# Kernel tuning notes

Measured on AMD Instinct MI355X. Metric: run time of the kernel, lower is better.

Reference implementation:

```python
import jax, jax.numpy as jnp
import numpy as np

NUM_MODULES, INP, OUT = 64, 256, 256
B, T = 2048, 64


def setup_inputs() -> dict:
    key = jax.random.key(0)
    k1, k2, k3, k4 = jax.random.split(key, 4)
    x = jax.random.normal(k1, (B, T, INP), dtype=jnp.float32)
    indices = jax.random.randint(k2, (B,), 0, NUM_MODULES)
    # torch.nn.Linear init: U(-1/sqrt(in), 1/sqrt(in)) for both weight and bias
    bound = 1.0 / np.sqrt(INP)
    W = jax.random.uniform(k3, (NUM_MODULES, OUT, INP), minval=-bound, maxval=bound, dtype=jnp.float32)
    b = jax.random.uniform(k4, (NUM_MODULES, OUT), minval=-bound, maxval=bound, dtype=jnp.float32)
    return {"x": x, "indices": indices, "W": W, "b": b}


def reference(x, indices, W, b):
    # Per-sample expert selection: gather each sample's weight/bias, batched matmul.
    Wg = W[indices]            # [B, OUT, INP]
    bg = b[indices]            # [B, OUT]
    y = jnp.einsum("bti,boi->bto", x, Wg) + bg[:, None, :]
    return y
```

## Files before the change

kernel.cpp:

```cpp
#include <hip/hip_runtime.h>
#include <hip/hip_bf16.h>

#define NMOD 64
#define INPD 256
#define OUTD 256
#define BATCH 2048
#define TT 64

typedef __attribute__((ext_vector_type(8))) short short8;
typedef __attribute__((ext_vector_type(4))) float floatx4;

__device__ __forceinline__ unsigned int pack2(float a, float b) {
    union { float f; unsigned int u; } ua, ub; ua.f = a; ub.f = b;
    unsigned int ra = ua.u + 0x7fffu + ((ua.u >> 16) & 1u);
    unsigned int rb = ub.u + 0x7fffu + ((ub.u >> 16) & 1u);
    return (ra >> 16) | (rb & 0xffff0000u);
}

__global__ __launch_bounds__(256) void conv_w_kernel(const float* __restrict__ W,
                                                     uint4* __restrict__ Wp) {
    int gid  = blockIdx.x * 256 + threadIdx.x;
    int lane = gid & 63;
    int frag = (gid >> 6) & 15;
    int ks   = (gid >> 10) & 7;
    int e    = gid >> 13;

    int n = (frag >> 3) * 128 + (frag & 7) * 16 + (lane & 15);
    int k = ks * 32 + (lane >> 4) * 8;

    const float* p = W + ((size_t)e * OUTD + n) * INPD + k;
    float4 v0 = *reinterpret_cast<const float4*>(p);
    float4 v1 = *reinterpret_cast<const float4*>(p + 4);
    Wp[gid] = make_uint4(pack2(v0.x, v0.y), pack2(v0.z, v0.w),
                         pack2(v1.x, v1.y), pack2(v1.z, v1.w));
}

template <bool PRECONV>
__global__ __launch_bounds__(256) void moe_gemm_kernel(
    const float* __restrict__ x, const int* __restrict__ idx,
    const void* __restrict__ Wsrc, const float* __restrict__ bias,
    float* __restrict__ y) {

    __shared__ unsigned short lx[TT * INPD];

    const int b    = blockIdx.x;
    const int tid  = threadIdx.x;
    const int lane = tid & 63;
    const int w    = tid >> 6;
    const int e    = idx[b];
    const int l15  = lane & 15;
    const int kq   = lane >> 4;

    const float4* xin = reinterpret_cast<const float4*>(x + (size_t)b * TT * INPD);
    char* lxc = reinterpret_cast<char*>(lx);
#pragma unroll
    for (int r = 0; r < 16; ++r) {
        int fid  = r * 256 + tid;
        float4 v = xin[fid];
        int t    = fid >> 6;
        int k    = (fid & 63) * 4;
        int byte = t * 512 + ((k * 2) ^ ((t & 7) << 4));
        __builtin_assume((byte & 7) == 0);
        *reinterpret_cast<uint2*>(lxc + byte) = make_uint2(pack2(v.x, v.y), pack2(v.z, v.w));
    }
    __syncthreads();

    floatx4 acc[4][4] = {};

#pragma unroll
    for (int ks = 0; ks < 8; ++ks) {
        short8 af[4];
#pragma unroll
        for (int mi = 0; mi < 4; ++mi) {
            int t    = mi * 16 + l15;
            int byte = t * 512 + ((ks * 64 + kq * 16) ^ ((t & 7) << 4));
            __builtin_assume((byte & 15) == 0);
            af[mi] = *reinterpret_cast<const short8*>(lxc + byte);
        }
        short8 bf[4];
        if (PRECONV) {
            const unsigned short* wp = reinterpret_cast<const unsigned short*>(Wsrc)
                + (((size_t)e * 8 + ks) << 13) + (w << 11) + (lane << 3);
#pragma unroll
            for (int ni = 0; ni < 4; ++ni)
                bf[ni] = *reinterpret_cast<const short8*>(wp + (ni << 9));
        } else {
            const float* Wf = reinterpret_cast<const float*>(Wsrc) + (size_t)e * OUTD * INPD;
#pragma unroll
            for (int ni = 0; ni < 4; ++ni) {
                int n = w * 64 + ni * 16 + l15;
                int k = ks * 32 + kq * 8;
                const float* p = Wf + (size_t)n * INPD + k;
                float4 v0 = *reinterpret_cast<const float4*>(p);
                float4 v1 = *reinterpret_cast<const float4*>(p + 4);
                union { short8 s; uint4 u; } cv;
                cv.u = make_uint4(pack2(v0.x, v0.y), pack2(v0.z, v0.w),
                                  pack2(v1.x, v1.y), pack2(v1.z, v1.w));
                bf[ni] = cv.s;
            }
        }
#pragma unroll
        for (int mi = 0; mi < 4; ++mi)
#pragma unroll
            for (int ni = 0; ni < 4; ++ni)
                acc[mi][ni] = __builtin_amdgcn_mfma_f32_16x16x32_bf16(
                    af[mi], bf[ni], acc[mi][ni], 0, 0, 0);
    }

    float bv[4];
#pragma unroll
    for (int ni = 0; ni < 4; ++ni)
        bv[ni] = bias[e * OUTD + w * 64 + ni * 16 + l15];

    float* yout = y + (size_t)b * TT * OUTD;
#pragma unroll
    for (int mi = 0; mi < 4; ++mi) {
#pragma unroll
        for (int ni = 0; ni < 4; ++ni) {
            int o = w * 64 + ni * 16 + l15;
#pragma unroll
            for (int r = 0; r < 4; ++r) {
                int t = mi * 16 + kq * 4 + r;
                yout[t * OUTD + o] = acc[mi][ni][r] + bv[ni];
            }
        }
    }
}

extern "C" void kernel_launch(void* const* d_in, const int* in_sizes, int n_in,
                              void* d_out, int out_size, void* d_ws, size_t ws_size,
                              hipStream_t stream) {
    const float* x    = (const float*)d_in[0];
    const int*   idx  = (const int*)d_in[1];
    const float* W    = (const float*)d_in[2];
    const float* bias = (const float*)d_in[3];
    float*       y    = (float*)d_out;

    const size_t w_elems      = (size_t)NMOD * OUTD * INPD;
    const size_t w_bf16_bytes = w_elems * sizeof(unsigned short);

    if (ws_size >= w_bf16_bytes) {
        conv_w_kernel<<<(unsigned)(w_elems / 8 / 256), 256, 0, stream>>>(
            W, reinterpret_cast<uint4*>(d_ws));
        moe_gemm_kernel<true><<<BATCH, 256, 0, stream>>>(x, idx, d_ws, bias, y);
    } else {
        moe_gemm_kernel<false><<<BATCH, 256, 0, stream>>>(x, idx, (const void*)W, bias, y);
    }
}
```

Before: 74.78 us.

## Load x directly into MFMA fragments, swap operands for vectorized output stores

Drops the LDS staging of the x tile and the block barrier. Each wave now loads and converts its A fragments from global memory directly, so every wave reloads the full x tile, which leans on L2/L1 for reuse. The MFMA operands are swapped so each lane holds four consecutive output columns, which turns the scalar output stores and bias loads into 16-byte vector accesses. A launch-bounds occupancy hint of 4 blocks is also added.

Measured after the change: 114.8 us. +53.5%, slower.

```diff
diff --git a/kernel.cpp b/kernel.cpp
--- a/kernel.cpp
+++ b/kernel.cpp
@@ -36,12 +36,10 @@
 }
 
 template <bool PRECONV>
-__global__ __launch_bounds__(256) void moe_gemm_kernel(
+__global__ __launch_bounds__(256, 4) void moe_gemm_kernel(
     const float* __restrict__ x, const int* __restrict__ idx,
     const void* __restrict__ Wsrc, const float* __restrict__ bias,
     float* __restrict__ y) {
-
-    __shared__ unsigned short lx[TT * INPD];
 
     const int b    = blockIdx.x;
     const int tid  = threadIdx.x;
@@ -51,19 +49,16 @@
     const int l15  = lane & 15;
     const int kq   = lane >> 4;
 
-    const float4* xin = reinterpret_cast<const float4*>(x + (size_t)b * TT * INPD);
-    char* lxc = reinterpret_cast<char*>(lx);
-#pragma unroll
-    for (int r = 0; r < 16; ++r) {
-        int fid  = r * 256 + tid;
-        float4 v = xin[fid];
-        int t    = fid >> 6;
-        int k    = (fid & 63) * 4;
-        int byte = t * 512 + ((k * 2) ^ ((t & 7) << 4));
-        __builtin_assume((byte & 7) == 0);
-        *reinterpret_cast<uint2*>(lxc + byte) = make_uint2(pack2(v.x, v.y), pack2(v.z, v.w));
+    const float* xa = x + (size_t)b * (TT * INPD) + (size_t)l15 * INPD + kq * 8;
+
+    const unsigned short* wp0 = nullptr;
+    const float* Wf = nullptr;
+    if (PRECONV) {
+        wp0 = reinterpret_cast<const unsigned short*>(Wsrc)
+              + ((size_t)e << 16) + (w << 11) + (lane << 3);
+    } else {
+        Wf = reinterpret_cast<const float*>(Wsrc) + (size_t)e * OUTD * INPD;
     }
-    __syncthreads();
 
     floatx4 acc[4][4] = {};
 
@@ -72,20 +67,21 @@
         short8 af[4];
 #pragma unroll
         for (int mi = 0; mi < 4; ++mi) {
-            int t    = mi * 16 + l15;
-            int byte = t * 512 + ((ks * 64 + kq * 16) ^ ((t & 7) << 4));
-            __builtin_assume((byte & 15) == 0);
-            af[mi] = *reinterpret_cast<const short8*>(lxc + byte);
+            const float* p = xa + mi * (16 * INPD) + ks * 32;
+            float4 v0 = *reinterpret_cast<const float4*>(p);
+            float4 v1 = *reinterpret_cast<const float4*>(p + 4);
+            union { short8 s; uint4 u; } cv;
+            cv.u = make_uint4(pack2(v0.x, v0.y), pack2(v0.z, v0.w),
+                              pack2(v1.x, v1.y), pack2(v1.z, v1.w));
+            af[mi] = cv.s;
         }
         short8 bf[4];
         if (PRECONV) {
-            const unsigned short* wp = reinterpret_cast<const unsigned short*>(Wsrc)
-                + (((size_t)e * 8 + ks) << 13) + (w << 11) + (lane << 3);
+            const unsigned short* wp = wp0 + ((size_t)ks << 13);
 #pragma unroll
             for (int ni = 0; ni < 4; ++ni)
                 bf[ni] = *reinterpret_cast<const short8*>(wp + (ni << 9));
         } else {
-            const float* Wf = reinterpret_cast<const float*>(Wsrc) + (size_t)e * OUTD * INPD;
 #pragma unroll
             for (int ni = 0; ni < 4; ++ni) {
                 int n = w * 64 + ni * 16 + l15;
@@ -104,26 +100,22 @@
 #pragma unroll
             for (int ni = 0; ni < 4; ++ni)
                 acc[mi][ni] = __builtin_amdgcn_mfma_f32_16x16x32_bf16(
-                    af[mi], bf[ni], acc[mi][ni], 0, 0, 0);
+                    bf[ni], af[mi], acc[mi][ni], 0, 0, 0);
     }
 
-    float bv[4];
+    const floatx4* bp = reinterpret_cast<const floatx4*>(bias + e * OUTD + w * 64) + kq;
+    floatx4 bv[4];
 #pragma unroll
     for (int ni = 0; ni < 4; ++ni)
-        bv[ni] = bias[e * OUTD + w * 64 + ni * 16 + l15];
+        bv[ni] = bp[ni * 4];
 
-    float* yout = y + (size_t)b * TT * OUTD;
+    float* yb = y + (size_t)b * (TT * OUTD) + (size_t)l15 * OUTD + w * 64 + kq * 4;
 #pragma unroll
     for (int mi = 0; mi < 4; ++mi) {
+        float* yrow = yb + mi * (16 * OUTD);
 #pragma unroll
-        for (int ni = 0; ni < 4; ++ni) {
-            int o = w * 64 + ni * 16 + l15;
-#pragma unroll
-            for (int r = 0; r < 4; ++r) {
-                int t = mi * 16 + kq * 4 + r;
-                yout[t * OUTD + o] = acc[mi][ni][r] + bv[ni];
-            }
-        }
+        for (int ni = 0; ni < 4; ++ni)
+            *reinterpret_cast<floatx4*>(yrow + ni * 16) = acc[mi][ni] + bv[ni];
     }
 }
 
```
